# Kernel tuning notes

Measured on AMD Instinct MI355X. Metric: run time of the kernel, lower is better.

The kernel has to match this reference:

```python
import jax, jax.numpy as jnp
import numpy as np

DIM = 512; HEADS = 8; DH = 64; M = 256; ITERS = 6; LN_EPS = 1e-5; RES_K = 33


def layernorm(x, g, b):
    mu = jnp.mean(x, -1, keepdims=True)
    var = jnp.mean((x - mu) ** 2, -1, keepdims=True)
    return (x - mu) * jax.lax.rsqrt(var + LN_EPS) * g + b


def moore_penrose_pinv(a, iters=ITERS):
    # Newton-Schulz iteration, matching nystrom_attention.moore_penrose_iter_pinv
    ab = jnp.abs(a)
    z = jnp.swapaxes(a, -1, -2) / (jnp.max(jnp.sum(ab, -1)) * jnp.max(jnp.sum(ab, -2)))
    I = jnp.eye(a.shape[-1], dtype=a.dtype)
    for _ in range(iters):
        az = a @ z
        z = 0.25 * z @ (13. * I - az @ (15. * I - az @ (7. * I - az)))
    return z


def dwconv2d(x, w, b, k):
    # x: [B,C,H,W], w: [C,1,k,k] depthwise
    C = x.shape[1]
    y = jax.lax.conv_general_dilated(x, w, (1, 1), [(k // 2, k // 2), (k // 2, k // 2)],
                                     feature_group_count=C,
                                     dimension_numbers=('NCHW', 'OIHW', 'NCHW'))
    return y + b[None, :, None, None]


def nystrom_attention(x, qkv_w, out_w, out_b, res_w):
    b, n, d = x.shape
    pad = (M - n % M) % M
    xp = jnp.pad(x, ((0, 0), (pad, 0), (0, 0)))  # pad at front, as in reference impl
    npd = n + pad
    qkv = xp @ qkv_w  # [b, npd, 3d]
    q, k, v = jnp.split(qkv, 3, axis=-1)
    to_heads = lambda t: t.reshape(b, npd, HEADS, DH).transpose(0, 2, 1, 3)  # bhnd
    q = to_heads(q) * (DH ** -0.5)
    k = to_heads(k)
    v = to_heads(v)
    l = npd // M  # tokens per landmark
    q_l = q.reshape(b, HEADS, M, l, DH).mean(3)  # [b,h,M,dh]
    k_l = k.reshape(b, HEADS, M, l, DH).mean(3)
    a1 = jax.nn.softmax(jnp.einsum('bhid,bhjd->bhij', q, k_l), axis=-1)    # [b,h,n,M]
    a2 = jax.nn.softmax(jnp.einsum('bhid,bhjd->bhij', q_l, k_l), axis=-1)  # [b,h,M,M]
    a3 = jax.nn.softmax(jnp.einsum('bhid,bhjd->bhij', q_l, k), axis=-1)    # [b,h,M,n]
    out = (a1 @ moore_penrose_pinv(a2)) @ (a3 @ v)  # [b,h,n,dh]
    # residual depthwise conv over sequence dim of v (channels = heads)
    res = jax.lax.conv_general_dilated(v, res_w, (1, 1), [(RES_K // 2, RES_K // 2), (0, 0)],
                                       feature_group_count=HEADS,
                                       dimension_numbers=('NCHW', 'OIHW', 'NCHW'))
    out = out + res
    out = out.transpose(0, 2, 1, 3).reshape(b, npd, d) @ out_w + out_b
    return out[:, -n:]


def _forward(x, fc1_w, fc1_b, cls_token,
             l1_norm_g, l1_norm_b, l1_qkv_w, l1_out_w, l1_out_b, l1_res_w,
             ppeg_w7, ppeg_b7, ppeg_w5, ppeg_b5, ppeg_w3, ppeg_b3,
             l2_norm_g, l2_norm_b, l2_qkv_w, l2_out_w, l2_out_b, l2_res_w,
             norm_g, norm_b, fc2_w, fc2_b):
    h = jax.nn.relu(x @ fc1_w + fc1_b)  # [B,N,C]
    B, N, C = h.shape
    Hs = int(np.ceil(np.sqrt(N)))
    add = Hs * Hs - N
    h = jnp.concatenate([h, h[:, :add]], axis=1)  # square padding
    cls = jnp.broadcast_to(cls_token, (B, 1, C))
    h = jnp.concatenate([cls, h], axis=1)  # [B, Hs*Hs+1, C]
    # TransLayer 1
    h = h + nystrom_attention(layernorm(h, l1_norm_g, l1_norm_b), l1_qkv_w, l1_out_w, l1_out_b, l1_res_w)
    # PPEG
    cls_t, feat = h[:, 0], h[:, 1:]
    cf = feat.transpose(0, 2, 1).reshape(B, C, Hs, Hs)
    y = cf + dwconv2d(cf, ppeg_w7, ppeg_b7, 7) + dwconv2d(cf, ppeg_w5, ppeg_b5, 5) + dwconv2d(cf, ppeg_w3, ppeg_b3, 3)
    h = jnp.concatenate([cls_t[:, None], y.reshape(B, C, Hs * Hs).transpose(0, 2, 1)], axis=1)
    # TransLayer 2
    h = h + nystrom_attention(layernorm(h, l2_norm_g, l2_norm_b), l2_qkv_w, l2_out_w, l2_out_b, l2_res_w)
    h = layernorm(h, norm_g, norm_b)[:, 0]
    return h @ fc2_w + fc2_b  # logits [B, n_classes]


def setup_inputs() -> dict:
    key = jax.random.key(0)
    ks = jax.random.split(key, 32)
    B, N, IN, C, NC = 1, 16384, 1024, 512, 4
    s = 0.02
    f32 = jnp.float32
    d = {}
    d['x'] = jax.random.normal(ks[0], (B, N, IN), f32)
    d['fc1_w'] = jax.random.normal(ks[1], (IN, C), f32) * s
    d['fc1_b'] = jnp.zeros((C,), f32)
    d['cls_token'] = jax.random.normal(ks[2], (1, 1, C), f32)
    for i, p in enumerate(['l1', 'l2']):
        kk = jax.random.split(ks[3 + i], 8)
        d[p + '_norm_g'] = jnp.ones((C,), f32)
        d[p + '_norm_b'] = jnp.zeros((C,), f32)
        d[p + '_qkv_w'] = jax.random.normal(kk[0], (C, 3 * C), f32) * s
        d[p + '_out_w'] = jax.random.normal(kk[1], (C, C), f32) * s
        d[p + '_out_b'] = jnp.zeros((C,), f32)
        d[p + '_res_w'] = jax.random.normal(kk[2], (HEADS, 1, RES_K, 1), f32) * s
    for i, k_sz in enumerate([7, 5, 3]):
        d[f'ppeg_w{k_sz}'] = jax.random.normal(ks[8 + i], (C, 1, k_sz, k_sz), f32) * s
        d[f'ppeg_b{k_sz}'] = jnp.zeros((C,), f32)
    d['norm_g'] = jnp.ones((C,), f32)
    d['norm_b'] = jnp.zeros((C,), f32)
    d['fc2_w'] = jax.random.normal(ks[12], (C, NC), f32) * s
    d['fc2_b'] = jnp.zeros((NC,), f32)
    return d


def reference(x, fc1_w, fc1_b, cls_token,
              l1_norm_g, l1_norm_b, l1_qkv_w, l1_out_w, l1_out_b, l1_res_w,
              ppeg_w7, ppeg_b7, ppeg_w5, ppeg_b5, ppeg_w3, ppeg_b3,
              l2_norm_g, l2_norm_b, l2_qkv_w, l2_out_w, l2_out_b, l2_res_w,
              norm_g, norm_b, fc2_w, fc2_b):
    return _forward(x, fc1_w, fc1_b, cls_token,
                    l1_norm_g, l1_norm_b, l1_qkv_w, l1_out_w, l1_out_b, l1_res_w,
                    ppeg_w7, ppeg_b7, ppeg_w5, ppeg_b5, ppeg_w3, ppeg_b3,
                    l2_norm_g, l2_norm_b, l2_qkv_w, l2_out_w, l2_out_b, l2_res_w,
                    norm_g, norm_b, fc2_w, fc2_b)
```

## Files before the change

### kernel.cpp

```cpp
#include <hip/hip_runtime.h>


#define NT 16385
#define NP 16640
#define PAD 255
#define CDIM 512
#define HEADS 8
#define DH 64
#define LM 256
#define LSEG 65

typedef unsigned short u16;
typedef unsigned int u32;
typedef __attribute__((ext_vector_type(8))) short bf16x8;
typedef __attribute__((ext_vector_type(4))) float f32x4;

__device__ __forceinline__ u16 f2b(float f){
  u32 u = __float_as_uint(f);
  u32 r = (u + 0x7FFFu + ((u >> 16) & 1u)) >> 16;
  return (u16)r;
}
__device__ __forceinline__ float b2f(u16 h){ return __uint_as_float(((u32)h) << 16); }

__device__ __forceinline__ void gload16(const u16* g, u16* l){
  __builtin_amdgcn_global_load_lds(
      (const __attribute__((address_space(1))) u32*)g,
      (__attribute__((address_space(3))) u32*)l, 16, 0, 0);
}

__device__ __forceinline__ int xcd_swz(int orig, int nwg){
  int qn = nwg >> 3, rn = nwg & 7;
  int xcd = orig & 7, sid = orig >> 3;
  return (xcd < rn ? xcd * (qn + 1) : rn * (qn + 1) + (xcd - rn) * qn) + sid;
}

__device__ __forceinline__ float wredSum(float v){
#pragma unroll
  for (int o = 32; o > 0; o >>= 1) v += __shfl_xor(v, o, 64);
  return v;
}
__device__ __forceinline__ float wredMax(float v){
#pragma unroll
  for (int o = 32; o > 0; o >>= 1) v = fmaxf(v, __shfl_xor(v, o, 64));
  return v;
}
__device__ __forceinline__ float bredSum(float v, float* sm){
  v = wredSum(v);
  int w = threadIdx.x >> 6, l = threadIdx.x & 63;
  __syncthreads();
  if (l == 0) sm[w] = v;
  __syncthreads();
  return sm[0] + sm[1] + sm[2] + sm[3];
}
__device__ __forceinline__ float bredMax(float v, float* sm){
  v = wredMax(v);
  int w = threadIdx.x >> 6, l = threadIdx.x & 63;
  __syncthreads();
  if (l == 0) sm[w] = v;
  __syncthreads();
  return fmaxf(fmaxf(sm[0], sm[1]), fmaxf(sm[2], sm[3]));
}

__global__ __launch_bounds__(256) void copy_cls_k(const float* __restrict__ cls,
                                                  float* __restrict__ h){
  h[threadIdx.x] = cls[threadIdx.x];
  h[threadIdx.x + 256] = cls[threadIdx.x + 256];
}
__global__ __launch_bounds__(256) void cvtbf_k(const float* __restrict__ in,
                                               u16* __restrict__ out, long long n){
  long long i = ((long long)blockIdx.x * 256 + threadIdx.x) * 4;
  long long stride = (long long)gridDim.x * 256 * 4;
  for (; i < n; i += stride){
    float4 v = *(const float4*)(in + i);
    out[i]     = f2b(v.x);
    out[i + 1] = f2b(v.y);
    out[i + 2] = f2b(v.z);
    out[i + 3] = f2b(v.w);
  }
}
__global__ __launch_bounds__(256) void tcbf_k(const float* __restrict__ in,
    u16* __restrict__ out, int R, int C, int ldin, int ldout,
    long long sIn, long long sOut){
  __shared__ float t[32][33];
  in += (long long)blockIdx.z * sIn; out += (long long)blockIdx.z * sOut;
  int c0 = blockIdx.x * 32, r0 = blockIdx.y * 32;
  int x = threadIdx.x & 31, y = threadIdx.x >> 5;
  for (int yy = y; yy < 32; yy += 8){
    int r = r0 + yy, c = c0 + x;
    if (r < R && c < C) t[yy][x] = in[(long long)r * ldin + c];
  }
  __syncthreads();
  for (int yy = y; yy < 32; yy += 8){
    int c = c0 + yy, r = r0 + x;
    if (c < C && r < R) out[(long long)c * ldout + r] = f2b(t[x][yy]);
  }
}

#define GB_STOREBF 1
#define GB_RELU    2
#define GB_ACCUM   4
#define GB_ATOMIC  8
#define GB_QSCALE  16
#define GB_SWZ     32

template<int DBUF>
__global__ __launch_bounds__(256) void gemmbf_k(
    const u16* __restrict__ A, const u16* __restrict__ B, void* __restrict__ Cv,
    int M, int N, int K, int lda, int ldb, int ldc,
    long long sA, long long sB, long long sC,
    const float* __restrict__ bias, const float* __restrict__ rowdiv, int sRow,
    float alpha, int flags, int ksplit, u16* __restrict__ vt)
{
  __shared__ __align__(16) u16 sh[DBUF ? 32768 : 16384];
  int zb = blockIdx.z / ksplit;
  int ks = blockIdx.z - zb * ksplit;
  A += (long long)zb * sA; B += (long long)zb * sB;
  float* Cf = (float*)Cv + (long long)zb * sC;
  u16*   Ch = (u16*)Cv + (long long)zb * sC;
  int klen = K / ksplit;
  int kbeg = ks * klen, kend = kbeg + klen;
  int tid = threadIdx.x;
  int w = tid >> 6, l = tid & 63;
  int row0, col0;
  if (flags & GB_SWZ){
    int gx = gridDim.x;
    int swz = xcd_swz(blockIdx.y * gx + blockIdx.x, gx * gridDim.y);
    row0 = (swz / gx) * 128; col0 = (swz % gx) * 128;
  } else {
    row0 = blockIdx.y * 128; col0 = blockIdx.x * 128;
  }
  int r8 = l >> 3;
  int csrc = ((l & 7) ^ r8) * 8;
  f32x4 acc[2][8];
#pragma unroll
  for (int i = 0; i < 2; i++)
#pragma unroll
    for (int j = 0; j < 8; j++) acc[i][j] = (f32x4){0.f, 0.f, 0.f, 0.f};

  int mrow = l & 15, q8 = l >> 4;

  auto STAGE = [&](int buf, int k0){
    u16* Asb = sh + buf * 16384;
    u16* Bsb = Asb + 8192;
#pragma unroll
    for (int c = 0; c < 4; c++){
      int r = w * 32 + c * 8;
      int gm = row0 + r + r8; if (gm >= M) gm = M - 1;
      gload16(A + (long long)gm * lda + k0 + csrc, &Asb[r * 64]);
      int gn = col0 + r + r8; if (gn >= N) gn = N - 1;
      gload16(B + (long long)gn * ldb + k0 + csrc, &Bsb[r * 64]);
    }
  };
  auto COMPUTE = [&](int buf){
    const u16* Asb = sh + buf * 16384;
    const u16* Bsb = Asb + 8192;
#pragma unroll
    for (int ks2 = 0; ks2 < 2; ks2++){
      int kc = ks2 * 4 + q8;
      bf16x8 af[2], bfr[8];
#pragma unroll
      for (int i = 0; i < 2; i++){
        int r = w * 32 + i * 16 + mrow;
        af[i] = *(const bf16x8*)&Asb[r * 64 + ((kc ^ (r & 7)) * 8)];
      }
#pragma unroll
      for (int j = 0; j < 8; j++){
        int r = j * 16 + mrow;
        bfr[j] = *(const bf16x8*)&Bsb[r * 64 + ((kc ^ (r & 7)) * 8)];
      }
#pragma unroll
      for (int i = 0; i < 2; i++)
#pragma unroll
        for (int j = 0; j < 8; j++)
          acc[i][j] = __builtin_amdgcn_mfma_f32_16x16x32_bf16(af[i], bfr[j], acc[i][j], 0, 0, 0);
    }
  };

  if constexpr (DBUF){
    STAGE(0, kbeg);
    __syncthreads();
    int cur = 0;
    for (int k0 = kbeg; k0 < kend; k0 += 64){
      if (k0 + 64 < kend) STAGE(cur ^ 1, k0 + 64);
      COMPUTE(cur);
      __syncthreads();
      cur ^= 1;
    }
  } else {
    for (int k0 = kbeg; k0 < kend; k0 += 64){
      STAGE(0, k0);
      __syncthreads();
      COMPUTE(0);
      __syncthreads();
    }
  }

  if (flags & GB_STOREBF){
#pragma unroll
    for (int p = 0; p < 2; p++){
      __syncthreads();
#pragma unroll
      for (int i = 0; i < 2; i++)
#pragma unroll
        for (int r = 0; r < 4; r++){
          int lrow = w * 32 + i * 16 + q8 * 4 + r;
          int gm = row0 + lrow;
          float rd = rowdiv ? rowdiv[(long long)zb * sRow + gm] : 1.f;
#pragma unroll
          for (int jj = 0; jj < 4; jj++){
            int j = p * 4 + jj;
            int gn = col0 + j * 16 + mrow;
            float v = alpha * acc[i][j][r];
            if ((flags & GB_QSCALE) && gn < 512) v *= 0.125f;
            if (rowdiv) v /= rd;
            if (bias) v += bias[gn];
            if (flags & GB_RELU) v = fmaxf(v, 0.f);
            sh[lrow * 72 + (j * 16 + mrow - p * 64)] = f2b(v);
          }
        }
      __syncthreads();
#pragma unroll
      for (int it = 0; it < 4; it++){
        int cidx = tid + it * 256;
        int rr = cidx >> 3, c8 = (cidx & 7) * 8;
        int gm = row0 + rr;
        if (gm < M)
          *(uint4*)(Ch + (long long)gm * ldc + col0 + p * 64 + c8) =
              *(const uint4*)&sh[rr * 72 + c8];
      }
    }
    if (vt && col0 >= 1024){
      int gc0 = col0 - 1024;
#pragma unroll
      for (int p = 0; p < 2; p++){
        __syncthreads();
#pragma unroll
        for (int i = 0; i < 2; i++)
#pragma unroll
          for (int r = 0; r < 4; r++){
            int lrow = w * 32 + i * 16 + q8 * 4 + r;
#pragma unroll
            for (int jj = 0; jj < 4; jj++){
              int j = p * 4 + jj;
              int lcol = j * 16 + mrow - p * 64;
              sh[lcol * 136 + lrow] = f2b(alpha * acc[i][j][r]);
            }
          }
        __syncthreads();
#pragma unroll
        for (int it = 0; it < 4; it++){
          int cidx = tid + it * 256;
          int cc = cidx >> 4, rc = (cidx & 15) * 8;
          *(uint4*)(vt + (long long)(gc0 + p * 64 + cc) * NP + row0 + rc) =
              *(const uint4*)&sh[cc * 136 + rc];
        }
      }
    }
    return;
  }

  if constexpr (DBUF){
    if (!(flags & GB_ATOMIC)){
      float* shf = (float*)sh;
#pragma unroll
      for (int p = 0; p < 2; p++){
        __syncthreads();
#pragma unroll
        for (int i = 0; i < 2; i++)
#pragma unroll
          for (int r = 0; r < 4; r++){
            int lrow = w * 32 + i * 16 + q8 * 4 + r;
            int gm = row0 + lrow;
            int gmc = (gm < M) ? gm : M - 1;
            float rd = rowdiv ? rowdiv[(long long)zb * sRow + gmc] : 1.f;
#pragma unroll
            for (int jj = 0; jj < 4; jj++){
              int j = p * 4 + jj;
              int gn = col0 + j * 16 + mrow;
              float v = alpha * acc[i][j][r];
              if ((flags & GB_QSCALE) && gn < 512) v *= 0.125f;
              if (rowdiv) v /= rd;
              if (bias) v += bias[gn];
              if (flags & GB_RELU) v = fmaxf(v, 0.f);
              shf[lrow * 68 + (j * 16 + mrow - p * 64)] = v;
            }
          }
        __syncthreads();
#pragma unroll
        for (int it = 0; it < 8; it++){
          int cidx = tid + it * 256;
          int rr = cidx >> 4, c4 = (cidx & 15) * 4;
          int gm = row0 + rr;
          if (gm >= M) continue;
          int gn = col0 + p * 64 + c4;
          if (gn + 3 < N){
            float4* dst = (float4*)(Cf + (long long)gm * ldc + gn);
            float4 vv = *(const float4*)&shf[rr * 68 + c4];
            if (flags & GB_ACCUM){
              float4 o = *dst;
              vv.x += o.x; vv.y += o.y; vv.z += o.z; vv.w += o.w;
            }
            *dst = vv;
          } else {
            for (int e = 0; e < 4; e++){
              if (gn + e >= N) break;
              float v = shf[rr * 68 + c4 + e];
              if (flags & GB_ACCUM) Cf[(long long)gm * ldc + gn + e] += v;
              else Cf[(long long)gm * ldc + gn + e] = v;
            }
          }
        }
      }
      return;
    }
  }

#pragma unroll
  for (int i = 0; i < 2; i++){
#pragma unroll
    for (int r = 0; r < 4; r++){
      int gm = row0 + w * 32 + i * 16 + q8 * 4 + r;
      if (gm >= M) continue;
      float rd = rowdiv ? rowdiv[(long long)zb * sRow + gm] : 1.f;
#pragma unroll
      for (int j = 0; j < 8; j++){
        int gn = col0 + j * 16 + mrow;
        if (gn >= N) continue;
        float v = alpha * acc[i][j][r];
        if ((flags & GB_QSCALE) && gn < 512) v *= 0.125f;
        if (rowdiv) v /= rd;
        if (bias) v += bias[gn];
        if (flags & GB_RELU) v = fmaxf(v, 0.f);
        long long ci = (long long)gm * ldc + gn;
        if (flags & GB_ATOMIC) atomicAdd(&Cf[ci], v);
        else if (flags & GB_ACCUM) Cf[ci] += v;
        else Cf[ci] = v;
      }
    }
  }
}

__device__ __forceinline__ void pinv_core(
    u16* lds, int cb, int rb, int head,
    const u16* __restrict__ Ah, const u16* __restrict__ Al,
    const u16* __restrict__ BTh, const u16* __restrict__ BTl,
    u16* __restrict__ Chh, u16* __restrict__ Cll,
    u16* __restrict__ CTh, u16* __restrict__ CTl,
    float* __restrict__ Cf,
    const u16* __restrict__ Avh, const u16* __restrict__ Avl,
    float dterm, float sterm, float eterm)
{
  long long off = (long long)head << 16;
  int tid = threadIdx.x, w = tid >> 6, l = tid & 63;
  int row0 = rb * 64, col0 = cb * 64;
  int r8 = l >> 3;
  int csrc = ((l & 7) ^ r8) * 8;
  int mrow = l & 15, q8 = l >> 4;
  f32x4 acc[4];
#pragma unroll
  for (int j = 0; j < 4; j++) acc[j] = (f32x4){0.f, 0.f, 0.f, 0.f};

  auto STAGE = [&](int buf, int k0){
    u16* Ash = lds + buf * 16384;
    u16* Asl = Ash + 4096;
    u16* Bsh = Ash + 8192;
    u16* Bsl = Ash + 12288;
#pragma unroll
    for (int c = 0; c < 2; c++){
      int r = w * 16 + c * 8;
      long long ga = off + (long long)(row0 + r + r8) * 256 + k0 + csrc;
      gload16(Ah + ga, &Ash[r * 64]);
      gload16(Al + ga, &Asl[r * 64]);
      long long gb = off + (long long)(col0 + r + r8) * 256 + k0 + csrc;
      gload16(BTh + gb, &Bsh[r * 64]);
      gload16(BTl + gb, &Bsl[r * 64]);
    }
  };
  auto COMPUTE = [&](int buf){
    const u16* Ash = lds + buf * 16384;
    const u16* Asl = Ash + 4096;
    const u16* Bsh = Ash + 8192;
    const u16* Bsl = Ash + 12288;
#pragma unroll
    for (int ks2 = 0; ks2 < 2; ks2++){
      int kc = ks2 * 4 + q8;
      bf16x8 ah, al, bh[4], bl[4];
      {
        int r = w * 16 + mrow;
        int idx = r * 64 + ((kc ^ (r & 7)) * 8);
        ah = *(const bf16x8*)&Ash[idx];
        al = *(const bf16x8*)&Asl[idx];
      }
#pragma unroll
      for (int j = 0; j < 4; j++){
        int r = j * 16 + mrow;
        int idx = r * 64 + ((kc ^ (r & 7)) * 8);
        bh[j] = *(const bf16x8*)&Bsh[idx];
        bl[j] = *(const bf16x8*)&Bsl[idx];
      }
#pragma unroll
      for (int j = 0; j < 4; j++){
        acc[j] = __builtin_amdgcn_mfma_f32_16x16x32_bf16(ah, bh[j], acc[j], 0, 0, 0);
        acc[j] = __builtin_amdgcn_mfma_f32_16x16x32_bf16(ah, bl[j], acc[j], 0, 0, 0);
        acc[j] = __builtin_amdgcn_mfma_f32_16x16x32_bf16(al, bh[j], acc[j], 0, 0, 0);
      }
    }
  };

  STAGE(0, 0);
  __syncthreads();
  int cur = 0;
  for (int k0 = 0; k0 < 256; k0 += 64){
    if (k0 + 64 < 256) STAGE(cur ^ 1, k0 + 64);
    COMPUTE(cur);
    __syncthreads();
    cur ^= 1;
  }

#pragma unroll
  for (int r = 0; r < 4; r++){
    int gm = row0 + w * 16 + q8 * 4 + r;
#pragma unroll
    for (int j = 0; j < 4; j++){
      int gn = col0 + j * 16 + mrow;
      float v = sterm * acc[j][r];
      if (Avh){
        long long ai = off + (long long)gm * 256 + gn;
        v += eterm * (b2f(Avh[ai]) + b2f(Avl[ai]));
      }
      if (gm == gn) v += dterm;
      acc[j][r] = v;
      long long ci = off + (long long)gm * 256 + gn;
      if (Cf) Cf[ci] = v;
      if (Chh){
        u16 hi = f2b(v);
        Chh[ci] = hi;
        Cll[ci] = f2b(v - b2f(hi));
      }
    }
  }
  if (CTh){
#pragma unroll
    for (int pass = 0; pass < 2; pass++){
      __syncthreads();
#pragma unroll
      for (int r = 0; r < 4; r++){
        int lm = w * 16 + q8 * 4 + r;
#pragma unroll
        for (int j = 0; j < 4; j++){
          int ln = j * 16 + mrow;
          float v = acc[j][r];
          u16 hi = f2b(v);
          lds[ln * 72 + lm] = (pass == 0) ? hi : f2b(v - b2f(hi));
        }
      }
      __syncthreads();
      u16* dst = (pass == 0) ? CTh : CTl;
#pragma unroll
      for (int it = 0; it < 2; it++){
        int cidx = tid + it * 256;
        int rr = cidx >> 3;
        int cc = (cidx & 7) * 8;
        *(uint4*)(dst + off + (long long)(col0 + rr) * 256 + row0 + cc) =
            *(const uint4*)&lds[rr * 72 + cc];
      }
    }
  }
}

__global__ __launch_bounds__(256) void pinvh_k(
    const u16* __restrict__ Ah, const u16* __restrict__ Al,
    const u16* __restrict__ BTh, const u16* __restrict__ BTl,
    u16* __restrict__ Chh, u16* __restrict__ Cll,
    u16* __restrict__ CTh, u16* __restrict__ CTl,
    float* __restrict__ Cf,
    const u16* __restrict__ Avh, const u16* __restrict__ Avl,
    float dterm, float sterm, float eterm)
{
  __shared__ __align__(16) u16 lds[32768];
  pinv_core(lds, blockIdx.x, blockIdx.y, blockIdx.z,
            Ah, Al, BTh, BTl, Chh, Cll, CTh, CTl, Cf, Avh, Avl,
            dterm, sterm, eterm);
}
__global__ __launch_bounds__(256) void pinv2_k(
    const u16* __restrict__ azh, const u16* __restrict__ azl,
    const u16* __restrict__ azTh, const u16* __restrict__ azTl,
    const u16* __restrict__ zh, const u16* __restrict__ zl,
    u16* __restrict__ tATh, u16* __restrict__ tATl,
    u16* __restrict__ zah, u16* __restrict__ zal)
{
  __shared__ __align__(16) u16 lds[32768];
  int head = blockIdx.z & 7;
  if (blockIdx.z < 8)
    pinv_core(lds, blockIdx.x, blockIdx.y, head, azh, azl, azTh, azTl,
              nullptr, nullptr, tATh, tATl, nullptr, azh, azl, 15.f, 1.f, -7.f);
  else
    pinv_core(lds, blockIdx.x, blockIdx.y, head, zh, zl, azTh, azTl,
              zah, zal, nullptr, nullptr, nullptr, nullptr, nullptr, 0.f, 1.f, 0.f);
}

#define GF_TRANSB 1
__global__ __launch_bounds__(256) void gemm_k(
    const float* __restrict__ A, const float* __restrict__ B, float* __restrict__ C,
    int M, int N, int K, int lda, int ldb, int ldc,
    long long sA, long long sB, long long sC, float alpha, int flags)
{
  __shared__ __align__(16) float As[16][68];
  __shared__ __align__(16) float Bs[16][68];
  int zb = blockIdx.z;
  A += (long long)zb * sA; B += (long long)zb * sB; C += (long long)zb * sC;
  int tid = threadIdx.x;
  int tx = tid & 15, ty = tid >> 4;
  int row0 = blockIdx.y * 64, col0 = blockIdx.x * 64;
  float acc[4][4] = {};
  for (int k0 = 0; k0 < K; k0 += 16){
#pragma unroll
    for (int i = 0; i < 4; i++){
      int idx = tid + i * 256;
      int mm = idx >> 4, kk = idx & 15;
      int gm = row0 + mm;
      As[kk][mm] = (gm < M) ? A[(long long)gm * lda + (k0 + kk)] : 0.f;
    }
    if (!(flags & GF_TRANSB)){
#pragma unroll
      for (int i = 0; i < 4; i++){
        int idx = tid + i * 256;
        int kk = idx >> 6, nn = idx & 63;
        int gn = col0 + nn;
        Bs[kk][nn] = (gn < N) ? B[(long long)(k0 + kk) * ldb + gn] : 0.f;
      }
    } else {
#pragma unroll
      for (int i = 0; i < 4; i++){
        int idx = tid + i * 256;
        int nn = idx >> 4, kk = idx & 15;
        int gn = col0 + nn;
        Bs[kk][nn] = (gn < N) ? B[(long long)gn * ldb + (k0 + kk)] : 0.f;
      }
    }
    __syncthreads();
#pragma unroll
    for (int kk = 0; kk < 16; kk++){
      float4 av = *(const float4*)&As[kk][ty * 4];
      float4 bv = *(const float4*)&Bs[kk][tx * 4];
      float a[4] = {av.x, av.y, av.z, av.w};
      float b[4] = {bv.x, bv.y, bv.z, bv.w};
#pragma unroll
      for (int i = 0; i < 4; i++)
#pragma unroll
        for (int j = 0; j < 4; j++)
          acc[i][j] = fmaf(a[i], b[j], acc[i][j]);
    }
    __syncthreads();
  }
#pragma unroll
  for (int i = 0; i < 4; i++){
    int gm = row0 + ty * 4 + i;
    if (gm >= M) continue;
#pragma unroll
    for (int j = 0; j < 4; j++){
      int gn = col0 + tx * 4 + j;
      if (gn >= N) continue;
      C[(long long)gm * ldc + gn] = alpha * acc[i][j];
    }
  }
}

__global__ __launch_bounds__(256) void fattn_k(
    const u16* __restrict__ Qp, int ldq,
    const u16* __restrict__ Kp, int ldk,
    const u16* __restrict__ Vp, int ldv,
    long long sQh, long long sKh, long long sVh,
    int keysPerChunk,
    u16* __restrict__ outB, int ldo,
    float* __restrict__ O3, float* __restrict__ ML3, int nchunks, int qrows,
    int mode)
{
  __shared__ u16 Qs[64][72];
  __shared__ u16 Ks[128][72];
  __shared__ u16 Vs[64][136];
  __shared__ u16 Ps[4][16][136];
  int tid = threadIdx.x;
  int w = tid >> 6, l = tid & 63;
  int mrow = l & 15, q8 = l >> 4;
  int gx = gridDim.x, gy = gridDim.y;
  int swz = xcd_swz((blockIdx.z * gy + blockIdx.y) * gx + blockIdx.x,
                    gx * gy * gridDim.z);
  int qt = swz % gx, t2 = swz / gx;
  int ch = t2 % gy, h = t2 / gy;
  const u16* Q = Qp + (long long)h * sQh;
  const u16* K = Kp + (long long)h * sKh;
  const u16* V = Vp + (long long)h * sVh;
  int q0 = qt * 64;
  for (int i = tid; i < 512; i += 256){
    int r = i >> 3, c = (i & 7) * 8;
    *(uint4*)&Qs[r][c] = *(const uint4*)(Q + (long long)(q0 + r) * ldq + c);
  }
  float m_st[4], l_st[4];
  f32x4 acc_o[4];
#pragma unroll
  for (int r = 0; r < 4; r++){
    m_st[r] = -3.0e38f; l_st[r] = 0.f;
    acc_o[r] = (f32x4){0.f, 0.f, 0.f, 0.f};
  }
  int kbase = ch * keysPerChunk;
  for (int kt = 0; kt < keysPerChunk; kt += 128){
    for (int i = tid; i < 1024; i += 256){
      int r = i >> 3, c = (i & 7) * 8;
      *(uint4*)&Ks[r][c] = *(const uint4*)(K + (long long)(kbase + kt + r) * ldk + c);
    }
    for (int i = tid; i < 1024; i += 256){
      int r = i >> 4, c = (i & 15) * 8;
      *(uint4*)&Vs[r][c] = *(const uint4*)(V + (long long)r * ldv + kbase + kt + c);
    }
    __syncthreads();
    f32x4 accs[8];
#pragma unroll
    for (int j = 0; j < 8; j++) accs[j] = (f32x4){0.f, 0.f, 0.f, 0.f};
#pragma unroll
    for (int ks2 = 0; ks2 < 2; ks2++){
      bf16x8 af = *(const bf16x8*)&Qs[w * 16 + mrow][ks2 * 32 + q8 * 8];
#pragma unroll
      for (int j = 0; j < 8; j++){
        bf16x8 bfv = *(const bf16x8*)&Ks[j * 16 + mrow][ks2 * 32 + q8 * 8];
        accs[j] = __builtin_amdgcn_mfma_f32_16x16x32_bf16(af, bfv, accs[j], 0, 0, 0);
      }
    }
#pragma unroll
    for (int r = 0; r < 4; r++){
      float tm = -3.0e38f;
#pragma unroll
      for (int j = 0; j < 8; j++) tm = fmaxf(tm, accs[j][r]);
      tm = fmaxf(tm, __shfl_xor(tm, 1, 64));
      tm = fmaxf(tm, __shfl_xor(tm, 2, 64));
      tm = fmaxf(tm, __shfl_xor(tm, 4, 64));
      tm = fmaxf(tm, __shfl_xor(tm, 8, 64));
      float mn = fmaxf(m_st[r], tm);
      float al = __expf(m_st[r] - mn);
      m_st[r] = mn;
      float rs = 0.f;
#pragma unroll
      for (int j = 0; j < 8; j++){
        float e = __expf(accs[j][r] - mn);
        accs[j][r] = e;
        rs += e;
      }
      rs += __shfl_xor(rs, 1, 64);
      rs += __shfl_xor(rs, 2, 64);
      rs += __shfl_xor(rs, 4, 64);
      rs += __shfl_xor(rs, 8, 64);
      l_st[r] = al * l_st[r] + rs;
#pragma unroll
      for (int j = 0; j < 4; j++) acc_o[j][r] *= al;
    }
#pragma unroll
    for (int j = 0; j < 8; j++)
#pragma unroll
      for (int r = 0; r < 4; r++)
        Ps[w][q8 * 4 + r][j * 16 + mrow] = f2b(accs[j][r]);
    __syncthreads();
#pragma unroll
    for (int kc = 0; kc < 4; kc++){
      bf16x8 af = *(const bf16x8*)&Ps[w][mrow][kc * 32 + q8 * 8];
#pragma unroll
      for (int j = 0; j < 4; j++){
        bf16x8 bfv = *(const bf16x8*)&Vs[j * 16 + mrow][kc * 32 + q8 * 8];
        acc_o[j] = __builtin_amdgcn_mfma_f32_16x16x32_bf16(af, bfv, acc_o[j], 0, 0, 0);
      }
    }
    __syncthreads();
  }
  if (mode == 0){
#pragma unroll
    for (int r = 0; r < 4; r++){
      int grow = q0 + w * 16 + q8 * 4 + r;
      float inv = 1.f / l_st[r];
#pragma unroll
      for (int j = 0; j < 4; j++)
        outB[(long long)grow * ldo + h * 64 + j * 16 + mrow] = f2b(acc_o[j][r] * inv);
    }
  } else {
#pragma unroll
    for (int r = 0; r < 4; r++){
      int row = q0 + w * 16 + q8 * 4 + r;
      long long b = ((long long)h * nchunks + ch) * qrows + row;
#pragma unroll
      for (int j = 0; j < 4; j++)
        O3[b * 64 + j * 16 + mrow] = acc_o[j][r];
      if (mrow == 0){
        ML3[b * 2] = m_st[r];
        ML3[b * 2 + 1] = l_st[r];
      }
    }
  }
}

__global__ __launch_bounds__(256) void comb3_k(
    const float* __restrict__ O3, const float* __restrict__ ML3,
    float* __restrict__ a3v)
{
  int h = blockIdx.y;
  int row = blockIdx.x * 4 + (threadIdx.x >> 6);
  int d = threadIdx.x & 63;
  float m = -3.0e38f;
  for (int c = 0; c < 13; c++)
    m = fmaxf(m, ML3[(((long long)h * 13 + c) * 256 + row) * 2]);
  float l = 0.f, o = 0.f;
  for (int c = 0; c < 13; c++){
    long long b = ((long long)h * 13 + c) * 256 + row;
    float wgt = __expf(ML3[b * 2] - m);
    l += wgt * ML3[b * 2 + 1];
    o += wgt * O3[b * 64 + d];
  }
  a3v[((long long)h * 256 + row) * 64 + d] = o / l;
}

__global__ __launch_bounds__(256) void ln_pad_k(
    const float* __restrict__ h, const float* __restrict__ g,
    const float* __restrict__ b, u16* __restrict__ out)
{
  __shared__ float sm[4];
  int row = blockIdx.x, tid = threadIdx.x;
  u16* o = out + (long long)row * CDIM;
  if (row < PAD){ o[tid] = 0; o[tid + 256] = 0; return; }
  const float* x = h + (long long)(row - PAD) * CDIM;
  float v0 = x[tid], v1 = x[tid + 256];
  float s = bredSum(v0 + v1, sm);
  float s2 = bredSum(v0 * v0 + v1 * v1, sm);
  float mean = s * (1.f / 512.f);
  float var = s2 * (1.f / 512.f) - mean * mean;
  float rstd = rsqrtf(var + 1e-5f);
  o[tid] = f2b((v0 - mean) * rstd * g[tid] + b[tid]);
  o[tid + 256] = f2b((v1 - mean) * rstd * g[tid + 256] + b[tid + 256]);
}

__global__ __launch_bounds__(256) void landmark_k(
    const u16* __restrict__ qkv, float* __restrict__ ql, float* __restrict__ kl,
    u16* __restrict__ qlh, u16* __restrict__ klh)
{
  int m = blockIdx.x * 2 + (threadIdx.x >> 7);
  int c8 = (threadIdx.x & 127) * 8;
  const u16* base = qkv + (long long)(m * LSEG) * 1536 + c8;
  float s[8] = {};
  for (int j = 0; j < LSEG; j++){
    uint4 pk = *(const uint4*)(base + (long long)j * 1536);
    const u16* pv = (const u16*)&pk;
#pragma unroll
    for (int e = 0; e < 8; e++) s[e] += b2f(pv[e]);
  }
#pragma unroll
  for (int e = 0; e < 8; e++){
    int col = c8 + e;
    float v = s[e] * (1.f / 65.f);
    int h = (col & 511) >> 6, d = col & 63;
    int idx = (h * LM + m) * DH + d;
    if (col < 512){ ql[idx] = v; qlh[idx] = f2b(v); }
    else          { kl[idx] = v; klh[idx] = f2b(v); }
  }
}

__global__ __launch_bounds__(256) void softmax256_k(float* __restrict__ S,
    u16* __restrict__ a2h, u16* __restrict__ a2l, float* __restrict__ scal)
{
  __shared__ float sm[4];
  int i = blockIdx.x, h = blockIdx.y, j = threadIdx.x;
  if (i == 0 && h == 0 && j < 2) scal[j] = 0.f;
  long long idx = ((long long)h * LM + i) * 256 + j;
  float v = S[idx];
  float m = bredMax(v, sm);
  float e = __expf(v - m);
  float s = bredSum(e, sm);
  float p = e / s;
  S[idx] = p;
  u16 hi = f2b(p);
  a2h[idx] = hi;
  a2l[idx] = f2b(p - b2f(hi));
}

__global__ __launch_bounds__(256) void pinv_scal_k(
    const float* __restrict__ a2, float* __restrict__ scal)
{
  __shared__ float sm[4];
  int h = blockIdx.x, i = threadIdx.x;
  const float* Ah = a2 + (long long)h * 65536;
  float rs = 0.f, cs = 0.f;
  for (int j = 0; j < 256; j++){
    rs += fabsf(Ah[i * 256 + j]);
    cs += fabsf(Ah[j * 256 + i]);
  }
  float rmax = bredMax(rs, sm);
  __syncthreads();
  float cmax = bredMax(cs, sm);
  if (i == 0){
    atomicMax((int*)&scal[0], __float_as_int(rmax));
    atomicMax((int*)&scal[1], __float_as_int(cmax));
  }
}

__global__ __launch_bounds__(256) void z0_k(
    const float* __restrict__ a2, const float* __restrict__ scal,
    u16* __restrict__ zh, u16* __restrict__ zl,
    u16* __restrict__ zTh, u16* __restrict__ zTl)
{
  int ri = blockIdx.x, h = blockIdx.y, j = threadIdx.x;
  float inv = 1.f / (scal[0] * scal[1]);
  long long base = ((long long)h * LM + ri) * 256;
  float v = a2[base + j] * inv;
  u16 hi = f2b(v), lo = f2b(v - b2f(hi));
  zTh[base + j] = hi; zTl[base + j] = lo;
  long long tb = ((long long)h * LM + j) * 256 + ri;
  zh[tb] = hi; zl[tb] = lo;
}

__global__ __launch_bounds__(256) void resconv_k(
    const u16* __restrict__ vT, const float* __restrict__ rw,
    u16* __restrict__ attn)
{
  int c = blockIdx.x * 256 + threadIdx.x;
  int s0 = blockIdx.y * 8;
  int h = c >> 6;
  float w[33];
#pragma unroll
  for (int t = 0; t < 33; t++) w[t] = rw[h * 33 + t];
  float vr[40];
  const u16* vrow = vT + (long long)c * NP;
  if (s0 >= 16 && s0 + 24 <= NP){
#pragma unroll
    for (int q = 0; q < 5; q++){
      uint4 pk = *(const uint4*)(vrow + s0 - 16 + q * 8);
      const u16* pv = (const u16*)&pk;
#pragma unroll
      for (int e = 0; e < 8; e++) vr[q * 8 + e] = b2f(pv[e]);
    }
  } else {
#pragma unroll
    for (int j = 0; j < 40; j++){
      int s = s0 - 16 + j;
      vr[j] = (s >= 0 && s < NP) ? b2f(vrow[s]) : 0.f;
    }
  }
#pragma unroll
  for (int i = 0; i < 8; i++){
    float a = 0.f;
#pragma unroll
    for (int t = 0; t < 33; t++) a = fmaf(vr[i + t], w[t], a);
    long long idx = (long long)(s0 + i) * CDIM + c;
    attn[idx] = f2b(b2f(attn[idx]) + a);
  }
}

__global__ __launch_bounds__(256) void transpose_k(
    const float* __restrict__ in, float* __restrict__ out, int R, int Cc)
{
  __shared__ float t[32][33];
  int bx = blockIdx.x * 32, by = blockIdx.y * 32;
  int x = threadIdx.x & 31, y4 = threadIdx.x >> 5;
  for (int yy = y4; yy < 32; yy += 8){
    int r = by + yy, c = bx + x;
    if (r < R && c < Cc) t[yy][x] = in[(long long)r * Cc + c];
  }
  __syncthreads();
  for (int yy = y4; yy < 32; yy += 8){
    int r = bx + yy, c = by + x;
    if (r < Cc && c < R) out[(long long)r * R + c] = t[x][yy];
  }
}

__global__ __launch_bounds__(256) void ppeg_k(
    const float* __restrict__ cf, float* __restrict__ yt,
    const float* __restrict__ w7, const float* __restrict__ b7,
    const float* __restrict__ w5, const float* __restrict__ b5,
    const float* __restrict__ w3, const float* __restrict__ b3)
{
  __shared__ float tile[22][136];
  __shared__ float wsh[84];
  int c = blockIdx.y;
  int ys = blockIdx.x * 16;
  int tid = threadIdx.x;
  const float* img = cf + (long long)c * 16384;
  if (tid < 49) wsh[tid] = w7[c * 49 + tid];
  else if (tid >= 64 && tid < 89) wsh[49 + tid - 64] = w5[c * 25 + (tid - 64)];
  else if (tid >= 96 && tid < 105) wsh[74 + tid - 96] = w3[c * 9 + (tid - 96)];
  else if (tid == 128) wsh[83] = b7[c] + b5[c] + b3[c];
  for (int i = tid; i < 22 * 134; i += 256){
    int yy = i / 134, xx = i - yy * 134;
    int gy = ys - 3 + yy, gx = xx - 3;
    tile[yy][xx] = (gy >= 0 && gy < 128 && gx >= 0 && gx < 128) ? img[gy * 128 + gx] : 0.f;
  }
  __syncthreads();
  int x = tid & 127;
  int yo = (tid >> 7) * 8;
  float acc[8];
#pragma unroll
  for (int i = 0; i < 8; i++) acc[i] = tile[yo + i + 3][x + 3] + wsh[83];
#pragma unroll
  for (int kx = 0; kx < 7; kx++){
    float col[14];
#pragma unroll
    for (int t = 0; t < 14; t++) col[t] = tile[yo + t][x + kx];
    float wc7[7];
#pragma unroll
    for (int ky = 0; ky < 7; ky++) wc7[ky] = wsh[ky * 7 + kx];
#pragma unroll
    for (int i = 0; i < 8; i++)
#pragma unroll
      for (int ky = 0; ky < 7; ky++)
        acc[i] = fmaf(col[i + ky], wc7[ky], acc[i]);
    if (kx >= 1 && kx <= 5){
      float wc5[5];
#pragma unroll
      for (int ky = 0; ky < 5; ky++) wc5[ky] = wsh[49 + ky * 5 + (kx - 1)];
#pragma unroll
      for (int i = 0; i < 8; i++)
#pragma unroll
        for (int ky = 0; ky < 5; ky++)
          acc[i] = fmaf(col[i + 1 + ky], wc5[ky], acc[i]);
    }
    if (kx >= 2 && kx <= 4){
      float wc3[3];
#pragma unroll
      for (int ky = 0; ky < 3; ky++) wc3[ky] = wsh[74 + ky * 3 + (kx - 2)];
#pragma unroll
      for (int i = 0; i < 8; i++)
#pragma unroll
        for (int ky = 0; ky < 3; ky++)
          acc[i] = fmaf(col[i + 2 + ky], wc3[ky], acc[i]);
    }
  }
  float* dst = yt + (long long)c * 16384 + (ys + yo) * 128 + x;
#pragma unroll
  for (int i = 0; i < 8; i++) dst[i * 128] = acc[i];
}

__global__ __launch_bounds__(256) void final_k(
    const float* __restrict__ h, const float* __restrict__ g,
    const float* __restrict__ b, const float* __restrict__ w,
    const float* __restrict__ bias, float* __restrict__ out)
{
  __shared__ float sm[4];
  __shared__ float pj[256][4];
  int tid = threadIdx.x;
  float v0 = h[tid], v1 = h[tid + 256];
  float s = bredSum(v0 + v1, sm);
  float s2 = bredSum(v0 * v0 + v1 * v1, sm);
  float mean = s * (1.f / 512.f);
  float var = s2 * (1.f / 512.f) - mean * mean;
  float rstd = rsqrtf(var + 1e-5f);
  float n0 = (v0 - mean) * rstd * g[tid] + b[tid];
  float n1 = (v1 - mean) * rstd * g[tid + 256] + b[tid + 256];
#pragma unroll
  for (int j = 0; j < 4; j++)
    pj[tid][j] = n0 * w[tid * 4 + j] + n1 * w[(tid + 256) * 4 + j];
  __syncthreads();
  if (tid < 4){
    float acc = 0.f;
    for (int k = 0; k < 256; k++) acc += pj[k][tid];
    out[tid] = acc + bias[tid];
  }
}

static inline void gemmbf(hipStream_t st, const u16* A, const u16* B, void* C,
                          int M, int N, int K, int lda, int ldb, int ldc,
                          long long sA, long long sB, long long sC, int batch,
                          const float* bias, const float* rowdiv, int sRow,
                          float alpha, int flags, int ksplit, u16* vt, int dbuf)
{
  dim3 grid((N + 127) / 128, (M + 127) / 128, batch * ksplit);
  if (dbuf)
    gemmbf_k<1><<<grid, 256, 0, st>>>(A, B, C, M, N, K, lda, ldb, ldc, sA, sB, sC,
                                      bias, rowdiv, sRow, alpha, flags, ksplit, vt);
  else
    gemmbf_k<0><<<grid, 256, 0, st>>>(A, B, C, M, N, K, lda, ldb, ldc, sA, sB, sC,
                                      bias, rowdiv, sRow, alpha, flags, ksplit, vt);
}

#define B_H     0LL
#define B_XQ    33556480LL
#define B_ATTN  50595840LL
#define B_QKV   67635200LL
#define B_VT    118753280LL
#define B_O3    135792640LL
#define B_ML3   142608384LL
#define B_QL    169871360LL
#define B_KL    170395648LL
#define B_QLH   170919936LL
#define B_KLH   171182080LL
#define B_A2    171444224LL
#define B_PV2   173541376LL
#define B_A3V   184027136LL
#define B_Z2    184551424LL
#define B_Z2T   185075712LL
#define B_SCAL  185604096LL
#define B_W1T   185604352LL
#define B_WQT   186652928LL
#define B_WOT   188225792LL
#define WS_REQ  188750080LL
#define MB1     1048576LL

extern "C" void kernel_launch(void* const* d_in, const int* in_sizes, int n_in,
                              void* d_out, int out_size, void* d_ws, size_t ws_size,
                              hipStream_t stream)
{
  (void)in_sizes; (void)n_in; (void)out_size;
  if (ws_size < (size_t)WS_REQ) return;

  const float* x      = (const float*)d_in[0];
  const float* fc1_w  = (const float*)d_in[1];
  const float* fc1_b  = (const float*)d_in[2];
  const float* cls    = (const float*)d_in[3];
  const float* l_ng[2]  = {(const float*)d_in[4],  (const float*)d_in[10]};
  const float* l_nb[2]  = {(const float*)d_in[5],  (const float*)d_in[11]};
  const float* l_qkv[2] = {(const float*)d_in[6],  (const float*)d_in[12]};
  const float* l_ow[2]  = {(const float*)d_in[7],  (const float*)d_in[13]};
  const float* l_ob[2]  = {(const float*)d_in[8],  (const float*)d_in[14]};
  const float* l_rw[2]  = {(const float*)d_in[9],  (const float*)d_in[15]};
  const float* w7 = (const float*)d_in[16];
  const float* b7 = (const float*)d_in[17];
  const float* w5 = (const float*)d_in[18];
  const float* b5 = (const float*)d_in[19];
  const float* w3 = (const float*)d_in[20];
  const float* b3 = (const float*)d_in[21];
  const float* norm_g = (const float*)d_in[22];
  const float* norm_b = (const float*)d_in[23];
  const float* fc2_w  = (const float*)d_in[24];
  const float* fc2_b  = (const float*)d_in[25];
  float* out = (float*)d_out;

  char* WB = (char*)d_ws;
  float* h    = (float*)(WB + B_H);
  u16*   xq   = (u16*)(WB + B_XQ);
  u16*   attnb= (u16*)(WB + B_ATTN);
  u16*   qkvb = (u16*)(WB + B_QKV);
  u16*   xb   = (u16*)(WB + B_QKV);
  float* cf   = (float*)(WB + B_QKV);
  float* yt   = (float*)(WB + B_QKV + 33554432LL);
  u16*   vT   = (u16*)(WB + B_VT);
  float* O3   = (float*)(WB + B_O3);
  float* ML3  = (float*)(WB + B_ML3);
  float* ql   = (float*)(WB + B_QL);
  float* kl   = (float*)(WB + B_KL);
  u16*   qlh  = (u16*)(WB + B_QLH);
  u16*   klh  = (u16*)(WB + B_KLH);
  float* a2   = (float*)(WB + B_A2);
  float* a3v  = (float*)(WB + B_A3V);
  float* Z2   = (float*)(WB + B_Z2);
  u16*   Z2T  = (u16*)(WB + B_Z2T);
  float* scal = (float*)(WB + B_SCAL);
  u16*   w1T  = (u16*)(WB + B_W1T);
  u16*   wqT  = (u16*)(WB + B_WQT);
  u16*   woT  = (u16*)(WB + B_WOT);

  u16* a2h  = (u16*)(WB + B_XQ + 0 * MB1);
  u16* a2l  = (u16*)(WB + B_XQ + 1 * MB1);
  u16* z0h  = (u16*)(WB + B_XQ + 2 * MB1);
  u16* z0l  = (u16*)(WB + B_XQ + 3 * MB1);
  u16* z0Th = (u16*)(WB + B_XQ + 4 * MB1);
  u16* z0Tl = (u16*)(WB + B_XQ + 5 * MB1);
  u16* z1h  = (u16*)(WB + B_XQ + 6 * MB1);
  u16* z1l  = (u16*)(WB + B_XQ + 7 * MB1);
  u16* z1Th = (u16*)(WB + B_XQ + 8 * MB1);
  u16* z1Tl = (u16*)(WB + B_XQ + 9 * MB1);
  u16* azh  = (u16*)(WB + B_XQ + 10 * MB1);
  u16* azl  = (u16*)(WB + B_XQ + 11 * MB1);
  u16* azTh = (u16*)(WB + B_XQ + 12 * MB1);
  u16* azTl = (u16*)(WB + B_XQ + 13 * MB1);
  u16* tATh = (u16*)(WB + B_XQ + 14 * MB1);
  u16* tATl = (u16*)(WB + B_XQ + 15 * MB1);
  u16* zah  = (u16*)(WB + B_PV2 + 0 * MB1);
  u16* zal  = (u16*)(WB + B_PV2 + 1 * MB1);
  float* zf = (float*)(WB + B_PV2 + 2 * MB1);

  copy_cls_k<<<1, 256, 0, stream>>>(cls, h);
  cvtbf_k<<<4096, 256, 0, stream>>>(x, xb, 16384LL * 1024);
  tcbf_k<<<dim3(16, 32, 1), 256, 0, stream>>>(fc1_w, w1T, 1024, 512, 512, 1024, 0, 0);
  gemmbf(stream, xb, w1T, h + CDIM, 16384, 512, 1024, 1024, 1024, 512,
         0, 0, 0, 1, fc1_b, nullptr, 0, 1.f, GB_RELU, 1, nullptr, 1);

  for (int L = 0; L < 2; L++){
    ln_pad_k<<<NP, 256, 0, stream>>>(h, l_ng[L], l_nb[L], xq);
    tcbf_k<<<dim3(48, 16, 1), 256, 0, stream>>>(l_qkv[L], wqT, 512, 1536, 1536, 512, 0, 0);
    gemmbf(stream, xq, wqT, qkvb, NP, 1536, 512, 512, 512, 1536,
           0, 0, 0, 1, nullptr, nullptr, 0, 1.f, GB_STOREBF | GB_QSCALE | GB_SWZ, 1, vT, 1);
    landmark_k<<<LM / 2, 256, 0, stream>>>(qkvb, ql, kl, qlh, klh);
    gemm_k<<<dim3(4, 4, 8), 256, 0, stream>>>(ql, kl, a2, LM, LM, DH, DH, DH, LM,
                                              16384, 16384, 65536, 1.f, GF_TRANSB);
    softmax256_k<<<dim3(LM, HEADS), 256, 0, stream>>>(a2, a2h, a2l, scal);
    pinv_scal_k<<<HEADS, 256, 0, stream>>>(a2, scal);
    z0_k<<<dim3(LM, HEADS), 256, 0, stream>>>(a2, scal, z0h, z0l, z0Th, z0Tl);
    u16 *zh = z0h, *zl = z0l, *zTh = z0Th, *zTl = z0Tl;
    u16 *nzh = z1h, *nzl = z1l, *nzTh = z1Th, *nzTl = z1Tl;
    dim3 pg(4, 4, HEADS), pg2(4, 4, 2 * HEADS);
    for (int it = 0; it < 6; it++){
      pinvh_k<<<pg, 256, 0, stream>>>(a2h, a2l, zTh, zTl,
                                      azh, azl, azTh, azTl, nullptr,
                                      nullptr, nullptr, 0.f, 1.f, 0.f);
      pinv2_k<<<pg2, 256, 0, stream>>>(azh, azl, azTh, azTl, zh, zl,
                                       tATh, tATl, zah, zal);
      pinvh_k<<<pg, 256, 0, stream>>>(zah, zal, tATh, tATl,
                                      nzh, nzl, nzTh, nzTl,
                                      (it == 5) ? zf : nullptr,
                                      zh, zl, 0.f, -0.25f, 3.25f);
      u16* t;
      t = zh; zh = nzh; nzh = t;   t = zl; zl = nzl; nzl = t;
      t = zTh; zTh = nzTh; nzTh = t; t = zTl; zTl = nzTl; nzTl = t;
    }
    fattn_k<<<dim3(4, 13, 8), 256, 0, stream>>>(
        qlh, 64, qkvb + 512, 1536, vT, NP,
        16384, 64, 64LL * NP, 1280,
        nullptr, 0, O3, ML3, 13, 256, 1);
    comb3_k<<<dim3(64, 8), 256, 0, stream>>>(O3, ML3, a3v);
    gemm_k<<<dim3(1, 4, 8), 256, 0, stream>>>(zf, a3v, Z2, LM, DH, LM, LM, DH, DH,
                                              65536, 16384, 16384, 1.f, 0);
    tcbf_k<<<dim3(2, 8, 8), 256, 0, stream>>>(Z2, Z2T, 256, 64, 64, 256, 16384, 16384);
    fattn_k<<<dim3(260, 1, 8), 256, 0, stream>>>(
        qkvb, 1536, klh, 64, Z2T, 256,
        64, 16384, 16384, 256,
        attnb, CDIM, nullptr, nullptr, 1, NP, 0);
    resconv_k<<<dim3(2, NP / 8), 256, 0, stream>>>(vT, l_rw[L], attnb);
    tcbf_k<<<dim3(16, 16, 1), 256, 0, stream>>>(l_ow[L], woT, 512, 512, 512, 512, 0, 0);
    gemmbf(stream, attnb + (long long)PAD * CDIM, woT, h, NT, CDIM, CDIM,
           CDIM, CDIM, CDIM, 0, 0, 0, 1, l_ob[L], nullptr, 0, 1.f, GB_ACCUM, 1, nullptr, 1);

    if (L == 0){
      transpose_k<<<dim3(16, 512), 256, 0, stream>>>(h + CDIM, cf, 16384, CDIM);
      ppeg_k<<<dim3(8, 512), 256, 0, stream>>>(cf, yt, w7, b7, w5, b5, w3, b3);
      transpose_k<<<dim3(512, 16), 256, 0, stream>>>(yt, h + CDIM, CDIM, 16384);
    }
  }

  final_k<<<1, 256, 0, stream>>>(h, norm_g, norm_b, fc2_w, fc2_b, out);
}
```

Measured before the change: 1.252 ms.

## Fuse residual depthwise conv into attention epilogue and skip redundant V store

The separate resconv kernel is removed. Its 33-tap sequence convolution over V is now computed in the epilogue of the final attention kernel, using a shared-memory window of transposed V loaded per query tile. This avoids a read-modify-write pass over the attention output. The GEMM store path also skips the row-major bf16 store for V columns when only the transposed copy is needed. MFMA sections get s_setprio hints. The fused epilogue adds LDS usage and per-thread register pressure (a 36-float window), which could lower occupancy of the attention kernel.

```diff
diff --git a/kernel.cpp b/kernel.cpp
--- a/kernel.cpp
+++ b/kernel.cpp
@@ -196,37 +196,39 @@
   }
 
   if (flags & GB_STOREBF){
-#pragma unroll
-    for (int p = 0; p < 2; p++){
-      __syncthreads();
-#pragma unroll
-      for (int i = 0; i < 2; i++)
-#pragma unroll
-        for (int r = 0; r < 4; r++){
-          int lrow = w * 32 + i * 16 + q8 * 4 + r;
-          int gm = row0 + lrow;
-          float rd = rowdiv ? rowdiv[(long long)zb * sRow + gm] : 1.f;
-#pragma unroll
-          for (int jj = 0; jj < 4; jj++){
-            int j = p * 4 + jj;
-            int gn = col0 + j * 16 + mrow;
-            float v = alpha * acc[i][j][r];
-            if ((flags & GB_QSCALE) && gn < 512) v *= 0.125f;
-            if (rowdiv) v /= rd;
-            if (bias) v += bias[gn];
-            if (flags & GB_RELU) v = fmaxf(v, 0.f);
-            sh[lrow * 72 + (j * 16 + mrow - p * 64)] = f2b(v);
+    if (!(vt && col0 >= 1024)){
+#pragma unroll
+      for (int p = 0; p < 2; p++){
+        __syncthreads();
+#pragma unroll
+        for (int i = 0; i < 2; i++)
+#pragma unroll
+          for (int r = 0; r < 4; r++){
+            int lrow = w * 32 + i * 16 + q8 * 4 + r;
+            int gm = row0 + lrow;
+            float rd = rowdiv ? rowdiv[(long long)zb * sRow + gm] : 1.f;
+#pragma unroll
+            for (int jj = 0; jj < 4; jj++){
+              int j = p * 4 + jj;
+              int gn = col0 + j * 16 + mrow;
+              float v = alpha * acc[i][j][r];
+              if ((flags & GB_QSCALE) && gn < 512) v *= 0.125f;
+              if (rowdiv) v /= rd;
+              if (bias) v += bias[gn];
+              if (flags & GB_RELU) v = fmaxf(v, 0.f);
+              sh[lrow * 72 + (j * 16 + mrow - p * 64)] = f2b(v);
+            }
           }
+        __syncthreads();
+#pragma unroll
+        for (int it = 0; it < 4; it++){
+          int cidx = tid + it * 256;
+          int rr = cidx >> 3, c8 = (cidx & 7) * 8;
+          int gm = row0 + rr;
+          if (gm < M)
+            *(uint4*)(Ch + (long long)gm * ldc + col0 + p * 64 + c8) =
+                *(const uint4*)&sh[rr * 72 + c8];
         }
-      __syncthreads();
-#pragma unroll
-      for (int it = 0; it < 4; it++){
-        int cidx = tid + it * 256;
-        int rr = cidx >> 3, c8 = (cidx & 7) * 8;
-        int gm = row0 + rr;
-        if (gm < M)
-          *(uint4*)(Ch + (long long)gm * ldc + col0 + p * 64 + c8) =
-              *(const uint4*)&sh[rr * 72 + c8];
       }
     }
     if (vt && col0 >= 1024){
@@ -574,12 +576,14 @@
     int keysPerChunk,
     u16* __restrict__ outB, int ldo,
     float* __restrict__ O3, float* __restrict__ ML3, int nchunks, int qrows,
-    int mode)
+    int mode, const u16* __restrict__ vTc, const float* __restrict__ rw)
 {
   __shared__ u16 Qs[64][72];
   __shared__ u16 Ks[128][72];
   __shared__ u16 Vs[64][136];
   __shared__ u16 Ps[4][16][136];
+  __shared__ __align__(16) u16 Cv[64][104];
+  __shared__ float wsm[33];
   int tid = threadIdx.x;
   int w = tid >> 6, l = tid & 63;
   int mrow = l & 15, q8 = l >> 4;
@@ -587,7 +591,7 @@
   int swz = xcd_swz((blockIdx.z * gy + blockIdx.y) * gx + blockIdx.x,
                     gx * gy * gridDim.z);
   int qt = swz % gx, t2 = swz / gx;
-  int ch = t2 % gy, h = t2 / gy;
+  int ch_ = t2 % gy, h = t2 / gy;
   const u16* Q = Qp + (long long)h * sQh;
   const u16* K = Kp + (long long)h * sKh;
   const u16* V = Vp + (long long)h * sVh;
@@ -596,6 +600,26 @@
     int r = i >> 3, c = (i & 7) * 8;
     *(uint4*)&Qs[r][c] = *(const uint4*)(Q + (long long)(q0 + r) * ldq + c);
   }
+  if (vTc){
+    if (tid < 33) wsm[tid] = rw[h * 33 + tid];
+    for (int i = tid; i < 64 * 12; i += 256){
+      int ch = i / 12, seg = i - ch * 12;
+      int p0 = seg * 8;
+      int row = q0 - 16 + p0;
+      const u16* src = vTc + (long long)(h * 64 + ch) * NP;
+      u16 tmp[8];
+      if (row >= 0 && row + 8 <= NP){
+        *(uint4*)tmp = *(const uint4*)(src + row);
+      } else {
+#pragma unroll
+        for (int e = 0; e < 8; e++){
+          int rr2 = row + e;
+          tmp[e] = (rr2 >= 0 && rr2 < NP) ? src[rr2] : (u16)0;
+        }
+      }
+      *(uint4*)&Cv[ch][p0] = *(const uint4*)tmp;
+    }
+  }
   float m_st[4], l_st[4];
   f32x4 acc_o[4];
 #pragma unroll
@@ -603,7 +627,7 @@
     m_st[r] = -3.0e38f; l_st[r] = 0.f;
     acc_o[r] = (f32x4){0.f, 0.f, 0.f, 0.f};
   }
-  int kbase = ch * keysPerChunk;
+  int kbase = ch_ * keysPerChunk;
   for (int kt = 0; kt < keysPerChunk; kt += 128){
     for (int i = tid; i < 1024; i += 256){
       int r = i >> 3, c = (i & 7) * 8;
@@ -617,6 +641,7 @@
     f32x4 accs[8];
 #pragma unroll
     for (int j = 0; j < 8; j++) accs[j] = (f32x4){0.f, 0.f, 0.f, 0.f};
+    __builtin_amdgcn_s_setprio(1);
 #pragma unroll
     for (int ks2 = 0; ks2 < 2; ks2++){
       bf16x8 af = *(const bf16x8*)&Qs[w * 16 + mrow][ks2 * 32 + q8 * 8];
@@ -626,6 +651,7 @@
         accs[j] = __builtin_amdgcn_mfma_f32_16x16x32_bf16(af, bfv, accs[j], 0, 0, 0);
       }
     }
+    __builtin_amdgcn_s_setprio(0);
 #pragma unroll
     for (int r = 0; r < 4; r++){
       float tm = -3.0e38f;
@@ -659,6 +685,7 @@
       for (int r = 0; r < 4; r++)
         Ps[w][q8 * 4 + r][j * 16 + mrow] = f2b(accs[j][r]);
     __syncthreads();
+    __builtin_amdgcn_s_setprio(1);
 #pragma unroll
     for (int kc = 0; kc < 4; kc++){
       bf16x8 af = *(const bf16x8*)&Ps[w][mrow][kc * 32 + q8 * 8];
@@ -668,22 +695,43 @@
         acc_o[j] = __builtin_amdgcn_mfma_f32_16x16x32_bf16(af, bfv, acc_o[j], 0, 0, 0);
       }
     }
+    __builtin_amdgcn_s_setprio(0);
     __syncthreads();
   }
   if (mode == 0){
-#pragma unroll
-    for (int r = 0; r < 4; r++){
-      int grow = q0 + w * 16 + q8 * 4 + r;
-      float inv = 1.f / l_st[r];
-#pragma unroll
-      for (int j = 0; j < 4; j++)
-        outB[(long long)grow * ldo + h * 64 + j * 16 + mrow] = f2b(acc_o[j][r] * inv);
+    float invr[4];
+#pragma unroll
+    for (int r = 0; r < 4; r++) invr[r] = 1.f / l_st[r];
+#pragma unroll
+    for (int j = 0; j < 4; j++){
+      int ch = j * 16 + mrow;
+      float conv[4] = {0.f, 0.f, 0.f, 0.f};
+      if (vTc){
+        int rr0 = w * 16 + q8 * 4;
+        float win[36];
+#pragma unroll
+        for (int t = 0; t < 36; t++) win[t] = b2f(Cv[ch][rr0 + t]);
+#pragma unroll
+        for (int r = 0; r < 4; r++){
+          float a = 0.f;
+#pragma unroll
+          for (int t = 0; t < 33; t++) a = fmaf(win[r + t], wsm[t], a);
+          conv[r] = a;
+        }
+      }
+#pragma unroll
+      for (int r = 0; r < 4; r++){
+        int grow = q0 + w * 16 + q8 * 4 + r;
+        u16 o16 = f2b(acc_o[j][r] * invr[r]);
+        outB[(long long)grow * ldo + h * 64 + ch] =
+            vTc ? f2b(b2f(o16) + conv[r]) : o16;
+      }
     }
   } else {
 #pragma unroll
     for (int r = 0; r < 4; r++){
       int row = q0 + w * 16 + q8 * 4 + r;
-      long long b = ((long long)h * nchunks + ch) * qrows + row;
+      long long b = ((long long)h * nchunks + ch_) * qrows + row;
 #pragma unroll
       for (int j = 0; j < 4; j++)
         O3[b * 64 + j * 16 + mrow] = acc_o[j][r];
@@ -810,43 +858,6 @@
   zTh[base + j] = hi; zTl[base + j] = lo;
   long long tb = ((long long)h * LM + j) * 256 + ri;
   zh[tb] = hi; zl[tb] = lo;
-}
-
-__global__ __launch_bounds__(256) void resconv_k(
-    const u16* __restrict__ vT, const float* __restrict__ rw,
-    u16* __restrict__ attn)
-{
-  int c = blockIdx.x * 256 + threadIdx.x;
-  int s0 = blockIdx.y * 8;
-  int h = c >> 6;
-  float w[33];
-#pragma unroll
-  for (int t = 0; t < 33; t++) w[t] = rw[h * 33 + t];
-  float vr[40];
-  const u16* vrow = vT + (long long)c * NP;
-  if (s0 >= 16 && s0 + 24 <= NP){
-#pragma unroll
-    for (int q = 0; q < 5; q++){
-      uint4 pk = *(const uint4*)(vrow + s0 - 16 + q * 8);
-      const u16* pv = (const u16*)&pk;
-#pragma unroll
-      for (int e = 0; e < 8; e++) vr[q * 8 + e] = b2f(pv[e]);
-    }
-  } else {
-#pragma unroll
-    for (int j = 0; j < 40; j++){
-      int s = s0 - 16 + j;
-      vr[j] = (s >= 0 && s < NP) ? b2f(vrow[s]) : 0.f;
-    }
-  }
-#pragma unroll
-  for (int i = 0; i < 8; i++){
-    float a = 0.f;
-#pragma unroll
-    for (int t = 0; t < 33; t++) a = fmaf(vr[i + t], w[t], a);
-    long long idx = (long long)(s0 + i) * CDIM + c;
-    attn[idx] = f2b(b2f(attn[idx]) + a);
-  }
 }
 
 __global__ __launch_bounds__(256) void transpose_k(
@@ -1107,7 +1118,7 @@
     fattn_k<<<dim3(4, 13, 8), 256, 0, stream>>>(
         qlh, 64, qkvb + 512, 1536, vT, NP,
         16384, 64, 64LL * NP, 1280,
-        nullptr, 0, O3, ML3, 13, 256, 1);
+        nullptr, 0, O3, ML3, 13, 256, 1, nullptr, nullptr);
     comb3_k<<<dim3(64, 8), 256, 0, stream>>>(O3, ML3, a3v);
     gemm_k<<<dim3(1, 4, 8), 256, 0, stream>>>(zf, a3v, Z2, LM, DH, LM, LM, DH, DH,
                                               65536, 16384, 16384, 1.f, 0);
@@ -1115,8 +1126,7 @@
     fattn_k<<<dim3(260, 1, 8), 256, 0, stream>>>(
         qkvb, 1536, klh, 64, Z2T, 256,
         64, 16384, 16384, 256,
-        attnb, CDIM, nullptr, nullptr, 1, NP, 0);
-    resconv_k<<<dim3(2, NP / 8), 256, 0, stream>>>(vT, l_rw[L], attnb);
+        attnb, CDIM, nullptr, nullptr, 1, NP, 0, vT, l_rw[L]);
     tcbf_k<<<dim3(16, 16, 1), 256, 0, stream>>>(l_ow[L], woT, 512, 512, 512, 512, 0, 0);
     gemmbf(stream, attnb + (long long)PAD * CDIM, woT, h, NT, CDIM, CDIM,
            CDIM, CDIM, CDIM, 0, 0, 0, 1, l_ob[L], nullptr, 0, 1.f, GB_ACCUM, 1, nullptr, 1);
```

New measurement: 1.255 ms. About the same (+0.2%).
